# Kernel tuning notes

Measured on AMD Instinct MI355X. Metric: run time of the kernel, lower is better.

## Reference

```python
import jax, jax.numpy as jnp
import numpy as np

B, D, H = 8192, 256, 1024


def setup_inputs() -> dict:
    key = jax.random.key(0)
    ks = jax.random.split(key, 24)
    glorot = lambda k, o, i: jax.random.uniform(k, (o, i), jnp.float32, -1.0, 1.0) * jnp.sqrt(6.0 / (o + i))
    inp = {
        'x': jax.random.normal(ks[0], (B, D), jnp.float32),
        'm': (jax.random.uniform(ks[1], (B, D)) < 0.8).astype(jnp.float32),  # binary observation mask
        'delta': jax.random.uniform(ks[2], (B, D), jnp.float32),             # nonnegative time gaps
        'h': jax.random.normal(ks[3], (B, H), jnp.float32),
        'x_last_obs': jax.random.normal(ks[4], (B, D), jnp.float32),
        'x_mean': jax.random.normal(ks[5], (D,), jnp.float32),
        'W_gamma_x': jax.random.uniform(ks[6], (D,), jnp.float32, 0.001, 0.01),
        'b_gamma_x': jnp.zeros((D,), jnp.float32),
        'W_gamma_h': glorot(ks[7], H, D), 'b_gamma_h': jnp.zeros((H,), jnp.float32),
        'W_xz': glorot(ks[8], H, D), 'W_hz': glorot(ks[9], H, H),
        'W_mz': glorot(ks[10], H, D), 'b_mz': jnp.zeros((H,), jnp.float32),
        'W_xr': glorot(ks[11], H, D), 'W_hr': glorot(ks[12], H, H),
        'W_mr': glorot(ks[13], H, D), 'b_mr': jnp.zeros((H,), jnp.float32),
        'W_xh': glorot(ks[14], H, D), 'W_hh': glorot(ks[15], H, H),
        'W_mh': glorot(ks[16], H, D), 'b_mh': jnp.zeros((H,), jnp.float32),
    }
    return inp


def reference(x, m, delta, h, x_last_obs, x_mean,
              W_gamma_x, b_gamma_x, W_gamma_h, b_gamma_h,
              W_xz, W_hz, W_mz, b_mz,
              W_xr, W_hr, W_mr, b_mr,
              W_xh, W_hh, W_mh, b_mh):
    # input decay (per-feature) and hidden decay (linear of delta)
    gamma_x = jnp.exp(-jax.nn.relu(delta * W_gamma_x + b_gamma_x))        # [B, D]
    gamma_h = jnp.exp(-jax.nn.relu(delta @ W_gamma_h.T + b_gamma_h))     # [B, H]
    # imputation
    x_last_obs_new = jnp.where(m > 0, x, x_last_obs)
    x_imputed = gamma_x * x_last_obs_new + (1.0 - gamma_x) * x_mean
    x_hat = m * x + (1.0 - m) * x_imputed
    h_decayed = gamma_h * h
    # GRU gates (eval mode: no recurrent dropout)
    z = jax.nn.sigmoid(x_hat @ W_xz.T + h_decayed @ W_hz.T + m @ W_mz.T + b_mz)
    r = jax.nn.sigmoid(x_hat @ W_xr.T + h_decayed @ W_hr.T + m @ W_mr.T + b_mr)
    h_tilde = jnp.tanh(x_hat @ W_xh.T + (r * h_decayed) @ W_hh.T + m @ W_mh.T + b_mh)
    h_new = (1.0 - z) * h_decayed + z * h_tilde
    return h_new, x_last_obs_new
```

## Files before the change

### kernel.cpp

```cpp
#include <hip/hip_runtime.h>
#include <cstdint>
#include <cstddef>

typedef unsigned short u16;
typedef __attribute__((ext_vector_type(8))) short s16x8;
typedef __attribute__((ext_vector_type(8))) u16 u16x8;
typedef __attribute__((ext_vector_type(4))) float f32x4;

#define DEV static __device__ __forceinline__
#define GPTR(p) (const __attribute__((address_space(1))) void*)(p)
#define LPTR(p) (__attribute__((address_space(3))) void*)(p)
#define SCHEDB __builtin_amdgcn_sched_barrier(0)
#define BAR __builtin_amdgcn_s_barrier()
#define SETP1 __builtin_amdgcn_s_setprio(1)
#define SETP0 __builtin_amdgcn_s_setprio(0)

DEV float b2f(u16 u) { union { unsigned i; float f; } c; c.i = ((unsigned)u) << 16; return c.f; }
DEV u16 f2b(float f) {
  union { float f; unsigned i; } c; c.f = f;
  unsigned r = (c.i + 0x7fffu + ((c.i >> 16) & 1u)) >> 16;
  return (u16)r;
}
DEV float sigm(float x) { return 1.0f / (1.0f + __expf(-x)); }

__global__ __launch_bounds__(256) void pack_w(
    const float* __restrict__ Wxz, const float* __restrict__ Whz, const float* __restrict__ Wmz,
    const float* __restrict__ Wxr, const float* __restrict__ Whr, const float* __restrict__ Wmr,
    const float* __restrict__ Wxh, const float* __restrict__ Whh, const float* __restrict__ Wmh,
    const float* __restrict__ Wgh,
    u16* __restrict__ WZR, u16* __restrict__ WH, u16* __restrict__ WGH)
{
  int t = blockIdx.x * 256 + threadIdx.x;
  const float* src;
  u16* dst;
  if (t < 589824) {
    int row = t / 192;
    int col = (t % 192) * 8;
    int rr = row & 1023;
    const float *wx, *wh, *wm;
    if (row < 1024)      { wx = Wxz; wh = Whz; wm = Wmz; }
    else if (row < 2048) { wx = Wxr; wh = Whr; wm = Wmr; }
    else                 { wx = Wxh; wh = Whh; wm = Wmh; }
    if (col < 256)       src = wx + rr * 256 + col;
    else if (col < 1280) src = wh + (size_t)rr * 1024 + (col - 256);
    else                 src = wm + rr * 256 + (col - 1280);
    dst = (row < 2048) ? (WZR + (size_t)row * 1536 + col)
                       : (WH + (size_t)(row - 2048) * 1536 + col);
  } else {
    int t2 = t - 589824;
    src = Wgh + t2 * 8;
    dst = WGH + t2 * 8;
  }
  f32x4 a = *(const f32x4*)src;
  f32x4 b = *(const f32x4*)(src + 4);
  u16x8 v;
#pragma unroll
  for (int j = 0; j < 4; ++j) { v[j] = f2b(a[j]); v[j + 4] = f2b(b[j]); }
  *(u16x8*)dst = v;
}

__global__ __launch_bounds__(256) void elem_k(
    const float* __restrict__ x, const float* __restrict__ m, const float* __restrict__ delta,
    const float* __restrict__ xlo, const float* __restrict__ x_mean,
    const float* __restrict__ Wgx, const float* __restrict__ bgx,
    u16* __restrict__ X1, u16* __restrict__ X2, u16* __restrict__ Dbf,
    float* __restrict__ out_xlo)
{
  int t = blockIdx.x * 256 + threadIdx.x;
  int row = t >> 5;
  int col = (t & 31) * 8;
  size_t base = (size_t)row * 256 + col;
  u16x8 vxhat, vm16, vd16;
  f32x4 vlnew[2];
#pragma unroll
  for (int half = 0; half < 2; ++half) {
    f32x4 vx = *(const f32x4*)(x + base + half * 4);
    f32x4 vm = *(const f32x4*)(m + base + half * 4);
    f32x4 vd = *(const f32x4*)(delta + base + half * 4);
    f32x4 vl = *(const f32x4*)(xlo + base + half * 4);
    f32x4 vmean = *(const f32x4*)(x_mean + col + half * 4);
    f32x4 vwg = *(const f32x4*)(Wgx + col + half * 4);
    f32x4 vbg = *(const f32x4*)(bgx + col + half * 4);
#pragma unroll
    for (int j = 0; j < 4; ++j) {
      float mf = vm[j];
      float lnew = (mf > 0.5f) ? vx[j] : vl[j];
      vlnew[half][j] = lnew;
      float gx = __expf(-fmaxf(vd[j] * vwg[j] + vbg[j], 0.0f));
      float ximp = gx * lnew + (1.0f - gx) * vmean[j];
      float xhat = mf * vx[j] + (1.0f - mf) * ximp;
      vxhat[half * 4 + j] = f2b(xhat);
      vm16[half * 4 + j] = f2b(mf);
      vd16[half * 4 + j] = f2b(vd[j]);
    }
  }
  size_t r1536 = (size_t)row * 1536;
  *(u16x8*)(X1 + r1536 + col) = vxhat;
  *(u16x8*)(X2 + r1536 + col) = vxhat;
  *(u16x8*)(X1 + r1536 + 1280 + col) = vm16;
  *(u16x8*)(X2 + r1536 + 1280 + col) = vm16;
  *(u16x8*)(Dbf + base) = vd16;
  *(f32x4*)(out_xlo + base) = vlnew[0];
  *(f32x4*)(out_xlo + base + 4) = vlnew[1];
}

template<int EPI, int GXL>
__global__ __launch_bounds__(256, 2) void gemm_bt(
    const u16* __restrict__ A, int K, const u16* __restrict__ W,
    const float* __restrict__ bias0, const float* __restrict__ bias1,
    const float* __restrict__ auxf,
    const u16* __restrict__ auxb,
    const u16* __restrict__ aux2b,
    u16* __restrict__ out0b,
    u16* __restrict__ out1b,
    float* __restrict__ outf)
{
  constexpr int GX = 1 << GXL;
  constexpr int SL = 128 * 32;
  __shared__ alignas(16) u16 As[4][SL];
  __shared__ alignas(16) u16 Bs[4][SL];

  const int tid = threadIdx.x;
  const int lane = tid & 63;
  const int wave = tid >> 6;
  const int wr = wave >> 1, wc = wave & 1;

  const int d = blockIdx.x;
  const int q = (int)gridDim.x >> 3;
  const int L = (d & 7) * q + (d >> 3);
  const int brow = (L >> GXL) * 128;
  const int bcol = (L & (GX - 1)) * 128;
  const int NT = K / 64;

  const int lr = lane & 15, g4 = lane >> 4;
  const int rc = (g4 ^ ((lr >> 1) & 3)) * 8;
  const int sr4 = lane >> 2;
  const int scs = ((lane & 3) ^ ((lane >> 3) & 3)) * 8;

  f32x4 acc[4][4];
#pragma unroll
  for (int i = 0; i < 4; ++i)
#pragma unroll
    for (int j = 0; j < 4; ++j) { f32x4 z0 = {0.f, 0.f, 0.f, 0.f}; acc[i][j] = z0; }

  const u16* aP0 = A + (size_t)(brow + wave * 16 + sr4) * K + scs;
  const u16* aP1 = aP0 + (size_t)64 * K;
  const u16* bP0 = W + (size_t)(bcol + wave * 16 + sr4) * K + scs;
  const u16* bP1 = bP0 + (size_t)64 * K;
  u16* ldsA = &As[0][0] + wave * 512;
  u16* ldsB = &Bs[0][0] + wave * 512;
  const u16* rdA = &As[0][0] + (wr * 64 + lr) * 32 + rc;
  const u16* rdB = &Bs[0][0] + (wc * 64 + lr) * 32 + rc;

  auto STAGE = [&](int slot, int koff) {
    __builtin_amdgcn_global_load_lds(GPTR(aP0 + koff), LPTR(ldsA + slot * SL), 16, 0, 0);
    __builtin_amdgcn_global_load_lds(GPTR(aP1 + koff), LPTR(ldsA + slot * SL + 2048), 16, 0, 0);
    __builtin_amdgcn_global_load_lds(GPTR(bP0 + koff), LPTR(ldsB + slot * SL), 16, 0, 0);
    __builtin_amdgcn_global_load_lds(GPTR(bP1 + koff), LPTR(ldsB + slot * SL + 2048), 16, 0, 0);
  };

  auto PHASE = [&](int slotR, int slotS, int koff, int stg, int vm) {
    s16x8 af[4], bf[4];
    const u16* pA = rdA + slotR * SL;
    const u16* pB = rdB + slotR * SL;
#pragma unroll
    for (int i = 0; i < 4; ++i) af[i] = *(const s16x8*)(pA + i * 512);
#pragma unroll
    for (int j = 0; j < 4; ++j) bf[j] = *(const s16x8*)(pB + j * 512);
    if (stg) STAGE(slotS, koff);
    SCHEDB;
    if (vm == 4) asm volatile("s_waitcnt vmcnt(4)" ::: "memory");
    else if (vm == 0) asm volatile("s_waitcnt vmcnt(0)" ::: "memory");
    BAR;
    asm volatile("s_waitcnt lgkmcnt(0)" ::: "memory");
    SCHEDB;
    SETP1;
#pragma unroll
    for (int i = 0; i < 4; ++i)
#pragma unroll
      for (int j = 0; j < 4; ++j)
        acc[i][j] = __builtin_amdgcn_mfma_f32_16x16x32_bf16(af[i], bf[j], acc[i][j], 0, 0, 0);
    SETP0;
  };

  STAGE(0, 0);
  STAGE(1, 32);
  asm volatile("s_waitcnt vmcnt(4)" ::: "memory");
  BAR;

  for (int kt = 0; kt < NT - 2; kt += 2) {
    PHASE(0, 2, 64, 1, 4);
    PHASE(1, 3, 96, 1, 4);
    PHASE(2, 0, 128, 1, 4);
    PHASE(3, 1, 160, 1, 4);
    aP0 += 128; aP1 += 128; bP0 += 128; bP1 += 128;
  }
  PHASE(0, 2, 64, 1, 4);
  PHASE(1, 3, 96, 1, 4);
  PHASE(2, 0, 0, 0, 0);
  PHASE(3, 0, 0, 0, -1);

  const int row0 = brow + wr * 64 + g4 * 4;
  const int col0 = bcol + wc * 64 + lr;
#pragma unroll
  for (int i = 0; i < 4; ++i) {
#pragma unroll
    for (int j = 0; j < 4; ++j) {
      int c_ = col0 + j * 16;
#pragma unroll
      for (int qq = 0; qq < 4; ++qq) {
        int r_ = row0 + i * 16 + qq;
        float v = acc[i][j][qq];
        if constexpr (EPI == 0) {
          float p = v + bias0[c_];
          float gh = __expf(-fmaxf(p, 0.0f));
          float hd = gh * auxf[(size_t)r_ * 1024 + c_];
          out0b[(size_t)r_ * 1536 + 256 + c_] = f2b(hd);
        } else if constexpr (EPI == 1) {
          if (c_ < 1024) {
            out0b[(size_t)r_ * 1024 + c_] = f2b(sigm(v + bias0[c_]));
          } else {
            int jc = c_ - 1024;
            float rg = sigm(v + bias1[jc]);
            float hd = b2f(auxb[(size_t)r_ * 1536 + 256 + jc]);
            out1b[(size_t)r_ * 1536 + 256 + jc] = f2b(rg * hd);
          }
        } else {
          float ht = tanhf(v + bias0[c_]);
          float zz = b2f(aux2b[(size_t)r_ * 1024 + c_]);
          float hd = b2f(auxb[(size_t)r_ * 1536 + 256 + c_]);
          outf[(size_t)r_ * 1024 + c_] = (1.0f - zz) * hd + zz * ht;
        }
      }
    }
  }
}

extern "C" void kernel_launch(void* const* d_in, const int* in_sizes, int n_in,
                              void* d_out, int out_size, void* d_ws, size_t ws_size,
                              hipStream_t stream)
{
  const float* x     = (const float*)d_in[0];
  const float* m     = (const float*)d_in[1];
  const float* delta = (const float*)d_in[2];
  const float* h     = (const float*)d_in[3];
  const float* xlo   = (const float*)d_in[4];
  const float* xmean = (const float*)d_in[5];
  const float* Wgx   = (const float*)d_in[6];
  const float* bgx   = (const float*)d_in[7];
  const float* Wgh   = (const float*)d_in[8];
  const float* bgh   = (const float*)d_in[9];
  const float* Wxz   = (const float*)d_in[10];
  const float* Whz   = (const float*)d_in[11];
  const float* Wmz   = (const float*)d_in[12];
  const float* bmz   = (const float*)d_in[13];
  const float* Wxr   = (const float*)d_in[14];
  const float* Whr   = (const float*)d_in[15];
  const float* Wmr   = (const float*)d_in[16];
  const float* bmr   = (const float*)d_in[17];
  const float* Wxh   = (const float*)d_in[18];
  const float* Whh   = (const float*)d_in[19];
  const float* Wmh   = (const float*)d_in[20];
  const float* bmh   = (const float*)d_in[21];

  u16* X1  = (u16*)d_ws;
  u16* X2  = X1 + (size_t)8192 * 1536;
  u16* Z   = X2 + (size_t)8192 * 1536;
  u16* WZR = Z  + (size_t)8192 * 1024;
  u16* WH  = WZR + (size_t)2048 * 1536;
  u16* Dbf = WH + (size_t)1024 * 1536;
  u16* WGH = Dbf + (size_t)8192 * 256;

  float* out_h   = (float*)d_out;
  float* out_xlo = out_h + (size_t)8192 * 1024;

  pack_w<<<2432, 256, 0, stream>>>(Wxz, Whz, Wmz, Wxr, Whr, Wmr, Wxh, Whh, Wmh, Wgh, WZR, WH, WGH);
  elem_k<<<1024, 256, 0, stream>>>(x, m, delta, xlo, xmean, Wgx, bgx, X1, X2, Dbf, out_xlo);
  gemm_bt<0, 3><<<512, 256, 0, stream>>>(
      Dbf, 256, WGH, bgh, nullptr, h, nullptr, nullptr, X1, nullptr, nullptr);
  gemm_bt<1, 4><<<1024, 256, 0, stream>>>(
      X1, 1536, WZR, bmz, bmr, nullptr, X1, nullptr, Z, X2, nullptr);
  gemm_bt<2, 3><<<512, 256, 0, stream>>>(
      X2, 1536, WH, bmh, nullptr, nullptr, X1, Z, nullptr, nullptr, out_h);
}
```

Before: 178.4 us.

## Use 256x128 block tiles with 8 waves and a three-stage LDS pipeline

Replaces the 128x128, 4-wave GEMM with a 256x128 tile computed by 8 waves, so each B tile loaded into LDS is shared by twice as many rows. K is now a template parameter and the loop is fully unrolled. The four-slot, two-phase pipeline becomes a three-slot ring with one barrier per 32-wide k step. This halves grid sizes, which cuts global traffic for the weights, but uses more LDS per block and may reduce occupancy and parallelism.

```diff
diff --git a/kernel.cpp b/kernel.cpp
--- a/kernel.cpp
+++ b/kernel.cpp
@@ -10,7 +10,6 @@
 #define DEV static __device__ __forceinline__
 #define GPTR(p) (const __attribute__((address_space(1))) void*)(p)
 #define LPTR(p) (__attribute__((address_space(3))) void*)(p)
-#define SCHEDB __builtin_amdgcn_sched_barrier(0)
 #define BAR __builtin_amdgcn_s_barrier()
 #define SETP1 __builtin_amdgcn_s_setprio(1)
 #define SETP0 __builtin_amdgcn_s_setprio(0)
@@ -104,9 +103,9 @@
   *(f32x4*)(out_xlo + base + 4) = vlnew[1];
 }
 
-template<int EPI, int GXL>
-__global__ __launch_bounds__(256, 2) void gemm_bt(
-    const u16* __restrict__ A, int K, const u16* __restrict__ W,
+template<int EPI, int KK, int GXL>
+__global__ __launch_bounds__(512, 4) void gemm256(
+    const u16* __restrict__ A, const u16* __restrict__ W,
     const float* __restrict__ bias0, const float* __restrict__ bias1,
     const float* __restrict__ auxf,
     const u16* __restrict__ auxb,
@@ -115,27 +114,21 @@
     u16* __restrict__ out1b,
     float* __restrict__ outf)
 {
+  constexpr int P = KK / 32;
   constexpr int GX = 1 << GXL;
-  constexpr int SL = 128 * 32;
-  __shared__ alignas(16) u16 As[4][SL];
-  __shared__ alignas(16) u16 Bs[4][SL];
-
-  const int tid = threadIdx.x;
-  const int lane = tid & 63;
-  const int wave = tid >> 6;
+  __shared__ alignas(16) u16 As[3][8192];
+  __shared__ alignas(16) u16 Bs[3][4096];
+
+  const int tid = threadIdx.x, lane = tid & 63, wave = tid >> 6;
   const int wr = wave >> 1, wc = wave & 1;
-
   const int d = blockIdx.x;
   const int q = (int)gridDim.x >> 3;
   const int L = (d & 7) * q + (d >> 3);
-  const int brow = (L >> GXL) * 128;
-  const int bcol = (L & (GX - 1)) * 128;
-  const int NT = K / 64;
-
+  const int brow = (L >> GXL) * 256, bcol = (L & (GX - 1)) * 128;
   const int lr = lane & 15, g4 = lane >> 4;
   const int rc = (g4 ^ ((lr >> 1) & 3)) * 8;
-  const int sr4 = lane >> 2;
-  const int scs = ((lane & 3) ^ ((lane >> 3) & 3)) * 8;
+  const int srow = tid >> 2;
+  const int scs = ((tid & 3) ^ ((srow >> 1) & 3)) * 8;
 
   f32x4 acc[4][4];
 #pragma unroll
@@ -143,37 +136,37 @@
 #pragma unroll
     for (int j = 0; j < 4; ++j) { f32x4 z0 = {0.f, 0.f, 0.f, 0.f}; acc[i][j] = z0; }
 
-  const u16* aP0 = A + (size_t)(brow + wave * 16 + sr4) * K + scs;
-  const u16* aP1 = aP0 + (size_t)64 * K;
-  const u16* bP0 = W + (size_t)(bcol + wave * 16 + sr4) * K + scs;
-  const u16* bP1 = bP0 + (size_t)64 * K;
-  u16* ldsA = &As[0][0] + wave * 512;
-  u16* ldsB = &Bs[0][0] + wave * 512;
-  const u16* rdA = &As[0][0] + (wr * 64 + lr) * 32 + rc;
-  const u16* rdB = &Bs[0][0] + (wc * 64 + lr) * 32 + rc;
-
-  auto STAGE = [&](int slot, int koff) {
-    __builtin_amdgcn_global_load_lds(GPTR(aP0 + koff), LPTR(ldsA + slot * SL), 16, 0, 0);
-    __builtin_amdgcn_global_load_lds(GPTR(aP1 + koff), LPTR(ldsA + slot * SL + 2048), 16, 0, 0);
-    __builtin_amdgcn_global_load_lds(GPTR(bP0 + koff), LPTR(ldsB + slot * SL), 16, 0, 0);
-    __builtin_amdgcn_global_load_lds(GPTR(bP1 + koff), LPTR(ldsB + slot * SL + 2048), 16, 0, 0);
+  const u16* aP = A + (size_t)(brow + srow) * KK + scs;
+  const u16* aQ = aP + (size_t)128 * KK;
+  const u16* bP = W + (size_t)(bcol + srow) * KK + scs;
+  u16* dA = &As[0][0] + tid * 8;
+  u16* dB = &Bs[0][0] + tid * 8;
+  const u16* rA = &As[0][0] + (wr * 64 + lr) * 32 + rc;
+  const u16* rB = &Bs[0][0] + (wc * 64 + lr) * 32 + rc;
+
+  auto STAGE = [&](int slot, int ko) {
+    __builtin_amdgcn_global_load_lds(GPTR(aP + ko), LPTR(dA + slot * 8192), 16, 0, 0);
+    __builtin_amdgcn_global_load_lds(GPTR(aQ + ko), LPTR(dA + slot * 8192 + 4096), 16, 0, 0);
+    __builtin_amdgcn_global_load_lds(GPTR(bP + ko), LPTR(dB + slot * 4096), 16, 0, 0);
   };
 
-  auto PHASE = [&](int slotR, int slotS, int koff, int stg, int vm) {
+  STAGE(0, 0);
+  STAGE(1, 32);
+  asm volatile("s_waitcnt vmcnt(3)" ::: "memory");
+  BAR;
+  asm volatile("" ::: "memory");
+
+#pragma unroll
+  for (int u = 0; u < P; ++u) {
+    const int sR = u % 3;
+    const int sS = (u + 2) % 3;
+    const int ko = ((u + 2 < P) ? (u + 2) : (P - 1)) * 32;
+    STAGE(sS, ko);
     s16x8 af[4], bf[4];
-    const u16* pA = rdA + slotR * SL;
-    const u16* pB = rdB + slotR * SL;
-#pragma unroll
-    for (int i = 0; i < 4; ++i) af[i] = *(const s16x8*)(pA + i * 512);
-#pragma unroll
-    for (int j = 0; j < 4; ++j) bf[j] = *(const s16x8*)(pB + j * 512);
-    if (stg) STAGE(slotS, koff);
-    SCHEDB;
-    if (vm == 4) asm volatile("s_waitcnt vmcnt(4)" ::: "memory");
-    else if (vm == 0) asm volatile("s_waitcnt vmcnt(0)" ::: "memory");
-    BAR;
-    asm volatile("s_waitcnt lgkmcnt(0)" ::: "memory");
-    SCHEDB;
+#pragma unroll
+    for (int i = 0; i < 4; ++i) af[i] = *(const s16x8*)(rA + sR * 8192 + i * 512);
+#pragma unroll
+    for (int j = 0; j < 4; ++j) bf[j] = *(const s16x8*)(rB + sR * 4096 + j * 512);
     SETP1;
 #pragma unroll
     for (int i = 0; i < 4; ++i)
@@ -181,24 +174,11 @@
       for (int j = 0; j < 4; ++j)
         acc[i][j] = __builtin_amdgcn_mfma_f32_16x16x32_bf16(af[i], bf[j], acc[i][j], 0, 0, 0);
     SETP0;
-  };
-
-  STAGE(0, 0);
-  STAGE(1, 32);
-  asm volatile("s_waitcnt vmcnt(4)" ::: "memory");
-  BAR;
-
-  for (int kt = 0; kt < NT - 2; kt += 2) {
-    PHASE(0, 2, 64, 1, 4);
-    PHASE(1, 3, 96, 1, 4);
-    PHASE(2, 0, 128, 1, 4);
-    PHASE(3, 1, 160, 1, 4);
-    aP0 += 128; aP1 += 128; bP0 += 128; bP1 += 128;
-  }
-  PHASE(0, 2, 64, 1, 4);
-  PHASE(1, 3, 96, 1, 4);
-  PHASE(2, 0, 0, 0, 0);
-  PHASE(3, 0, 0, 0, -1);
+    asm volatile("s_waitcnt vmcnt(3) lgkmcnt(0)" ::: "memory");
+    BAR;
+    asm volatile("" ::: "memory");
+  }
+  asm volatile("s_waitcnt vmcnt(0)" ::: "memory");
 
   const int row0 = brow + wr * 64 + g4 * 4;
   const int col0 = bcol + wc * 64 + lr;
@@ -276,10 +256,10 @@
 
   pack_w<<<2432, 256, 0, stream>>>(Wxz, Whz, Wmz, Wxr, Whr, Wmr, Wxh, Whh, Wmh, Wgh, WZR, WH, WGH);
   elem_k<<<1024, 256, 0, stream>>>(x, m, delta, xlo, xmean, Wgx, bgx, X1, X2, Dbf, out_xlo);
-  gemm_bt<0, 3><<<512, 256, 0, stream>>>(
-      Dbf, 256, WGH, bgh, nullptr, h, nullptr, nullptr, X1, nullptr, nullptr);
-  gemm_bt<1, 4><<<1024, 256, 0, stream>>>(
-      X1, 1536, WZR, bmz, bmr, nullptr, X1, nullptr, Z, X2, nullptr);
-  gemm_bt<2, 3><<<512, 256, 0, stream>>>(
-      X2, 1536, WH, bmh, nullptr, nullptr, X1, Z, nullptr, nullptr, out_h);
-}
+  gemm256<0, 256, 3><<<256, 512, 0, stream>>>(
+      Dbf, WGH, bgh, nullptr, h, nullptr, nullptr, X1, nullptr, nullptr);
+  gemm256<1, 1536, 4><<<512, 512, 0, stream>>>(
+      X1, WZR, bmz, bmr, nullptr, X1, nullptr, Z, X2, nullptr);
+  gemm256<2, 1536, 3><<<256, 512, 0, stream>>>(
+      X2, WH, bmh, nullptr, nullptr, X1, Z, nullptr, nullptr, out_h);
+}
```

After: 163.5 us. -8.4%, faster.
